# Kernel tuning notes

Hardware: AMD Instinct MI355X
Metric: run time of the kernel (lower is better)

## Reference

```python
import jax, jax.numpy as jnp
import numpy as np

NUM_EMBEDDINGS = 1024
EMBEDDING_DIM = 256
BETA = 0.25


def setup_inputs() -> dict:
    key = jax.random.key(0)
    k1, k2 = jax.random.split(key)
    inputs = jax.random.normal(k1, (32, EMBEDDING_DIM, 64, 64), dtype=jnp.float32)
    # codebook init: uniform(-1/K, 1/K), matching nn.Embedding init in the module
    embedding = jax.random.uniform(
        k2, (NUM_EMBEDDINGS, EMBEDDING_DIM), dtype=jnp.float32,
        minval=-1.0 / NUM_EMBEDDINGS, maxval=1.0 / NUM_EMBEDDINGS)
    return {"inputs": inputs, "embedding": embedding, "beta": BETA}


def reference(inputs, embedding, beta):
    # inputs: [B, D, H, W] -> [B, H, W, D]
    x = jnp.transpose(inputs, (0, 2, 3, 1))
    in_shape = x.shape
    flat = x.reshape(-1, embedding.shape[1])  # [N, D]
    dist = (jnp.sum(flat * flat, axis=1, keepdims=True)
            + jnp.sum(embedding * embedding, axis=1)
            - 2.0 * flat @ embedding.T)
    codebook_indices = jnp.argmin(dist, axis=1)  # [N]
    quantized = embedding[codebook_indices].reshape(in_shape)  # [B,H,W,D]
    sg = jax.lax.stop_gradient
    e_latent_loss = beta * jnp.mean((sg(quantized) - x) ** 2)
    q_latent_loss = jnp.mean((quantized - sg(x)) ** 2)
    loss = e_latent_loss + q_latent_loss
    # straight-through estimator
    quantized_st = x + sg(quantized - x)
    return loss, jnp.transpose(quantized_st, (0, 3, 1, 2))
```

## Files before the change

### kernel.cpp

```cpp
#include <hip/hip_runtime.h>


#define DIN 256

typedef __attribute__((ext_vector_type(8))) short short8;
typedef __attribute__((ext_vector_type(4))) float float4v;
typedef __attribute__((ext_vector_type(4))) unsigned short ushort4v;

static __device__ __forceinline__ unsigned short f2bf(float f) {
  unsigned int u = __float_as_uint(f);
  unsigned int r = (u + 0x7fffu + ((u >> 16) & 1u)) >> 16;
  return (unsigned short)r;
}

__global__ void vq_prep(const float* __restrict__ e,
                        unsigned short* __restrict__ e_pre,
                        float* __restrict__ norms) {
  int wave = threadIdx.x >> 6, lane = threadIdx.x & 63;
  int k = blockIdx.x * 4 + wave;
  const float4v* src = (const float4v*)(e + k * DIN);
  float4v v = src[lane];
  float ss = v[0]*v[0] + v[1]*v[1] + v[2]*v[2] + v[3]*v[3];
  ushort4v pk;
  pk[0] = f2bf(v[0]); pk[1] = f2bf(v[1]); pk[2] = f2bf(v[2]); pk[3] = f2bf(v[3]);
  int t = k >> 5, kL = k & 31;
  int cc = lane >> 1, half = lane & 1;
  int s = cc ^ (kL & 7);
  *(ushort4v*)(e_pre + t * 8192 + kL * 256 + s * 8 + half * 4) = pk;
  #pragma unroll
  for (int m = 1; m < 64; m <<= 1) ss += __shfl_xor(ss, m, 64);
  if (lane == 0) norms[k] = ss;
}

#define BARRIER_RAW() do { asm volatile("" ::: "memory"); \
  __builtin_amdgcn_s_barrier(); asm volatile("" ::: "memory"); } while (0)

__global__ void __launch_bounds__(256, 2)
vq_main(const float* __restrict__ xin, const float* __restrict__ e_fp,
        const unsigned short* __restrict__ e_pre,
        const float* __restrict__ norms,
        float* __restrict__ out, float* __restrict__ loss_acc) {
  __shared__ char smem[65536];
  float* qs  = (float*)smem;
  float* nrm = (float*)(smem + 32768);
  float* xna = (float*)(smem + 36864);
  int*   fi  = (int*)(smem + 37888);
  float* prt = (float*)(smem + 38912);

  const int tid  = threadIdx.x;
  const int wave = tid >> 6, lane = tid & 63;
  const int m16  = lane & 15, quad = lane >> 4;
  const int line0 = blockIdx.x * 4;
  const int line  = line0 + wave;
  const float* xl = xin + (line >> 6) * 1048576 + (line & 63) * 64;

  auto stage = [&](int t, int buf) {
    const char* src = (const char*)e_pre + t * 16384;
    char* dst = smem + buf * 16384;
    #pragma unroll
    for (int j = 0; j < 4; ++j) {
      int off = j * 4096 + tid * 16;
      __builtin_amdgcn_global_load_lds(
          (const __attribute__((address_space(1))) unsigned int*)(src + off),
          (__attribute__((address_space(3))) unsigned int*)(dst + off),
          16, 0, 0);
    }
  };
  stage(0, 0);

  nrm[tid]       = norms[tid];
  nrm[tid + 256] = norms[tid + 256];
  nrm[tid + 512] = norms[tid + 512];
  nrm[tid + 768] = norms[tid + 768];

  short8 areg[32];
  {
    float ssq[4] = {0.0f, 0.0f, 0.0f, 0.0f};
    #pragma unroll
    for (int i = 0; i < 4; ++i) {
      const float* p = xl + i * 16 + m16;
      #pragma unroll
      for (int kk = 0; kk < 8; ++kk) {
        int dbase = kk * 32 + quad * 8;
        short8 pk;
        #pragma unroll
        for (int ii = 0; ii < 8; ++ii) {
          float xv = p[(dbase + ii) * 4096];
          ssq[i] += xv * xv;
          pk[ii] = (short)f2bf(xv);
        }
        areg[i * 8 + kk] = pk;
      }
    }
    #pragma unroll
    for (int i = 0; i < 4; ++i) {
      float s = ssq[i];
      s += __shfl_xor(s, 16, 64);
      s += __shfl_xor(s, 32, 64);
      if (quad == 0) xna[wave * 64 + i * 16 + m16] = s;
    }
  }

  float bestv[4][4];
  int   besti[4][4];
  #pragma unroll
  for (int i = 0; i < 4; ++i)
    #pragma unroll
    for (int r = 0; r < 4; ++r) { bestv[i][r] = INFINITY; besti[i][r] = 0; }

  for (int t = 0; t < 32; ++t) {
    if (t < 31) {
      stage(t + 1, (t + 1) & 1);
      asm volatile("s_waitcnt vmcnt(4)" ::: "memory");
    } else {
      asm volatile("s_waitcnt vmcnt(0)" ::: "memory");
    }
    BARRIER_RAW();
    const unsigned short* eb = (const unsigned short*)(smem + (t & 1) * 16384);
    #pragma unroll
    for (int j = 0; j < 2; ++j) {
      int cL = j * 16 + m16;
      float4v a0 = (float4v)(0.0f), a1 = (float4v)(0.0f);
      float4v a2 = (float4v)(0.0f), a3 = (float4v)(0.0f);
      #pragma unroll
      for (int kk = 0; kk < 8; ++kk) {
        short8 bfr = *(const short8*)(eb + cL * 256 + 8 * ((kk * 4 + quad) ^ (cL & 7)));
        a0 = __builtin_amdgcn_mfma_f32_16x16x32_bf16(areg[kk],      bfr, a0, 0, 0, 0);
        a1 = __builtin_amdgcn_mfma_f32_16x16x32_bf16(areg[8 + kk],  bfr, a1, 0, 0, 0);
        a2 = __builtin_amdgcn_mfma_f32_16x16x32_bf16(areg[16 + kk], bfr, a2, 0, 0, 0);
        a3 = __builtin_amdgcn_mfma_f32_16x16x32_bf16(areg[24 + kk], bfr, a3, 0, 0, 0);
      }
      int col = t * 32 + cL;
      float nj = nrm[col];
      #pragma unroll
      for (int r = 0; r < 4; ++r) {
        float s0 = nj - 2.0f * a0[r];
        if (s0 < bestv[0][r]) { bestv[0][r] = s0; besti[0][r] = col; }
        float s1 = nj - 2.0f * a1[r];
        if (s1 < bestv[1][r]) { bestv[1][r] = s1; besti[1][r] = col; }
        float s2 = nj - 2.0f * a2[r];
        if (s2 < bestv[2][r]) { bestv[2][r] = s2; besti[2][r] = col; }
        float s3 = nj - 2.0f * a3[r];
        if (s3 < bestv[3][r]) { bestv[3][r] = s3; besti[3][r] = col; }
      }
    }
    BARRIER_RAW();
  }

  #pragma unroll
  for (int msk = 1; msk <= 8; msk <<= 1) {
    #pragma unroll
    for (int i = 0; i < 4; ++i)
      #pragma unroll
      for (int r = 0; r < 4; ++r) {
        float ov = __shfl_xor(bestv[i][r], msk, 64);
        int   oi = __shfl_xor(besti[i][r], msk, 64);
        if (ov < bestv[i][r] || (ov == bestv[i][r] && oi < besti[i][r])) {
          bestv[i][r] = ov; besti[i][r] = oi;
        }
      }
  }

  float lsum = 0.0f;
  if (m16 == 0) {
    #pragma unroll
    for (int i = 0; i < 4; ++i)
      #pragma unroll
      for (int r = 0; r < 4; ++r) {
        int row = wave * 64 + i * 16 + quad * 4 + r;
        fi[row] = besti[i][r];
        lsum += bestv[i][r] + xna[row];
      }
  }
  #pragma unroll
  for (int msk = 1; msk < 64; msk <<= 1) lsum += __shfl_xor(lsum, msk, 64);
  if (lane == 0) prt[wave] = lsum;
  __syncthreads();
  if (tid == 0)
    atomicAdd(loss_acc, prt[0] + prt[1] + prt[2] + prt[3]);

  const int b0 = line0 >> 6, h0 = line0 & 63;
  float* out1 = out + 1 + b0 * 1048576 + h0 * 64;
  const int myidx = fi[tid];
  const float* er = e_fp + myidx * 256;
  __syncthreads();
  for (int q = 0; q < 4; ++q) {
    if (q) __syncthreads();
    #pragma unroll
    for (int c = 0; c < 16; ++c) {
      float4v qv = *(const float4v*)(er + q * 64 + c * 4);
      qs[(c * 4 + 0) * 256 + tid] = qv[0];
      qs[(c * 4 + 1) * 256 + tid] = qv[1];
      qs[(c * 4 + 2) * 256 + tid] = qv[2];
      qs[(c * 4 + 3) * 256 + tid] = qv[3];
    }
    __syncthreads();
    #pragma unroll
    for (int it = 0; it < 16; ++it) {
      int dl = it * 4 + wave;
      float4v ov = *(const float4v*)(qs + dl * 256 + lane * 4);
      *(float4v*)(out1 + (q * 64 + dl) * 4096 + lane * 4) = ov;
    }
  }
}

__global__ void vq_fin(const float* __restrict__ loss_acc,
                       const float* __restrict__ beta,
                       float* __restrict__ out) {
  out[0] = (1.0f + beta[0]) * loss_acc[0] / 33554432.0f;
}

extern "C" void kernel_launch(void* const* d_in, const int* in_sizes, int n_in,
                              void* d_out, int out_size, void* d_ws, size_t ws_size,
                              hipStream_t stream) {
  const float* xin  = (const float*)d_in[0];
  const float* emb  = (const float*)d_in[1];
  const float* beta = (const float*)d_in[2];
  float* out = (float*)d_out;
  float* loss_acc = (float*)d_ws;
  float* norms = (float*)((char*)d_ws + 4096);
  unsigned short* e_pre = (unsigned short*)((char*)d_ws + 8192);

  hipMemsetAsync(d_ws, 0, 4, stream);
  vq_prep<<<256, 256, 0, stream>>>(emb, e_pre, norms);
  vq_main<<<512, 256, 0, stream>>>(xin, emb, e_pre, norms, out, loss_acc);
  vq_fin<<<1, 1, 0, stream>>>(loss_acc, beta, out);
}
```

Measured before the change: 360.7 us.

## Split gather into separate scatter kernel using transposed codebook in LDS

Splits the fused argmin/gather kernel in two. The argmin kernel now loads x with coalesced per-lane reads, restages it through a swizzled LDS buffer to build the MFMA fragments, and writes the chosen indices to a global buffer. A new scatter kernel keeps a transposed fp32 codebook slice in LDS and writes the NCHW output directly, with no per-row gather. This targets the strided x loads and the LDS transpose stage for the output, at the cost of an extra launch and an index round-trip through global memory.

```diff
diff --git a/kernel.cpp b/kernel.cpp
--- a/kernel.cpp
+++ b/kernel.cpp
@@ -6,6 +6,7 @@
 typedef __attribute__((ext_vector_type(8))) short short8;
 typedef __attribute__((ext_vector_type(4))) float float4v;
 typedef __attribute__((ext_vector_type(4))) unsigned short ushort4v;
+typedef __attribute__((ext_vector_type(4))) int int4v;
 
 static __device__ __forceinline__ unsigned short f2bf(float f) {
   unsigned int u = __float_as_uint(f);
@@ -15,7 +16,8 @@
 
 __global__ void vq_prep(const float* __restrict__ e,
                         unsigned short* __restrict__ e_pre,
-                        float* __restrict__ norms) {
+                        float* __restrict__ norms,
+                        float* __restrict__ eT) {
   int wave = threadIdx.x >> 6, lane = threadIdx.x & 63;
   int k = blockIdx.x * 4 + wave;
   const float4v* src = (const float4v*)(e + k * DIN);
@@ -28,6 +30,9 @@
   int s = cc ^ (kL & 7);
   *(ushort4v*)(e_pre + t * 8192 + kL * 256 + s * 8 + half * 4) = pk;
   #pragma unroll
+  for (int ii = 0; ii < 4; ++ii)
+    eT[(lane * 4 + ii) * 1024 + k] = v[ii];
+  #pragma unroll
   for (int m = 1; m < 64; m <<= 1) ss += __shfl_xor(ss, m, 64);
   if (lane == 0) norms[k] = ss;
 }
@@ -36,22 +41,18 @@
   __builtin_amdgcn_s_barrier(); asm volatile("" ::: "memory"); } while (0)
 
 __global__ void __launch_bounds__(256, 2)
-vq_main(const float* __restrict__ xin, const float* __restrict__ e_fp,
-        const unsigned short* __restrict__ e_pre,
-        const float* __restrict__ norms,
-        float* __restrict__ out, float* __restrict__ loss_acc) {
-  __shared__ char smem[65536];
-  float* qs  = (float*)smem;
-  float* nrm = (float*)(smem + 32768);
-  float* xna = (float*)(smem + 36864);
-  int*   fi  = (int*)(smem + 37888);
-  float* prt = (float*)(smem + 38912);
+vq_argmin(const float* __restrict__ xin,
+          const unsigned short* __restrict__ e_pre,
+          const float* __restrict__ norms,
+          int* __restrict__ fig, float* __restrict__ loss_acc) {
+  __shared__ __align__(16) char smem[69648];
+  float* nrm = (float*)(smem + 65536);
+  float* prt = (float*)(smem + 69632);
 
   const int tid  = threadIdx.x;
   const int wave = tid >> 6, lane = tid & 63;
   const int m16  = lane & 15, quad = lane >> 4;
-  const int line0 = blockIdx.x * 4;
-  const int line  = line0 + wave;
+  const int line = blockIdx.x * 4 + wave;
   const float* xl = xin + (line >> 6) * 1048576 + (line & 63) * 64;
 
   auto stage = [&](int t, int buf) {
@@ -68,38 +69,35 @@
   };
   stage(0, 0);
 
-  nrm[tid]       = norms[tid];
-  nrm[tid + 256] = norms[tid + 256];
-  nrm[tid + 512] = norms[tid + 512];
-  nrm[tid + 768] = norms[tid + 768];
-
+  *(float4v*)(nrm + tid * 4) = *(const float4v*)(norms + tid * 4);
+
+  unsigned short* xsw = (unsigned short*)(smem + 32768 + wave * 8192);
   short8 areg[32];
-  {
-    float ssq[4] = {0.0f, 0.0f, 0.0f, 0.0f};
-    #pragma unroll
-    for (int i = 0; i < 4; ++i) {
-      const float* p = xl + i * 16 + m16;
-      #pragma unroll
-      for (int kk = 0; kk < 8; ++kk) {
-        int dbase = kk * 32 + quad * 8;
-        short8 pk;
-        #pragma unroll
-        for (int ii = 0; ii < 8; ++ii) {
-          float xv = p[(dbase + ii) * 4096];
-          ssq[i] += xv * xv;
-          pk[ii] = (short)f2bf(xv);
-        }
-        areg[i * 8 + kk] = pk;
-      }
-    }
-    #pragma unroll
-    for (int i = 0; i < 4; ++i) {
-      float s = ssq[i];
-      s += __shfl_xor(s, 16, 64);
-      s += __shfl_xor(s, 32, 64);
-      if (quad == 0) xna[wave * 64 + i * 16 + m16] = s;
-    }
-  }
+  float ssq = 0.0f;
+  #pragma unroll
+  for (int q = 0; q < 4; ++q) {
+    #pragma unroll
+    for (int c = 0; c < 8; ++c) {
+      short8 pk;
+      #pragma unroll
+      for (int ii = 0; ii < 8; ++ii) {
+        float xv = xl[(q * 64 + c * 8 + ii) * 4096 + lane];
+        ssq += xv * xv;
+        pk[ii] = (short)f2bf(xv);
+      }
+      *(short8*)(xsw + lane * 64 + ((c ^ (lane & 7)) * 8)) = pk;
+    }
+    #pragma unroll
+    for (int i = 0; i < 4; ++i)
+      #pragma unroll
+      for (int kl = 0; kl < 2; ++kl) {
+        int r = i * 16 + m16;
+        int cl = kl * 4 + quad;
+        areg[i * 8 + q * 2 + kl] =
+            *(short8*)(xsw + r * 64 + ((cl ^ (r & 7)) * 8));
+      }
+  }
+  asm volatile("s_waitcnt lgkmcnt(0)" ::: "memory");
 
   float bestv[4][4];
   int   besti[4][4];
@@ -161,15 +159,15 @@
       }
   }
 
-  float lsum = 0.0f;
+  float lsum = ssq;
   if (m16 == 0) {
     #pragma unroll
     for (int i = 0; i < 4; ++i)
       #pragma unroll
       for (int r = 0; r < 4; ++r) {
-        int row = wave * 64 + i * 16 + quad * 4 + r;
-        fi[row] = besti[i][r];
-        lsum += bestv[i][r] + xna[row];
+        int row = i * 16 + quad * 4 + r;
+        fig[line * 64 + row] = besti[i][r];
+        lsum += bestv[i][r];
       }
   }
   #pragma unroll
@@ -178,28 +176,50 @@
   __syncthreads();
   if (tid == 0)
     atomicAdd(loss_acc, prt[0] + prt[1] + prt[2] + prt[3]);
-
-  const int b0 = line0 >> 6, h0 = line0 & 63;
-  float* out1 = out + 1 + b0 * 1048576 + h0 * 64;
-  const int myidx = fi[tid];
-  const float* er = e_fp + myidx * 256;
+}
+
+__global__ void __launch_bounds__(256, 3)
+vq_scatter(const float* __restrict__ eT, const int* __restrict__ fig,
+           float* __restrict__ out) {
+  __shared__ __align__(16) char smem[49152];
+  float* eTl = (float*)smem;
+  int*   fil = (int*)(smem + 32768);
+  const int tid = threadIdx.x;
+  const int b = blockIdx.x >> 5, dc = blockIdx.x & 31;
+
+  const char* s0 = (const char*)eT + dc * 32768;
+  #pragma unroll
+  for (int j = 0; j < 8; ++j) {
+    int off = j * 4096 + tid * 16;
+    __builtin_amdgcn_global_load_lds(
+        (const __attribute__((address_space(1))) unsigned int*)(s0 + off),
+        (__attribute__((address_space(3))) unsigned int*)(smem + off),
+        16, 0, 0);
+  }
+  const char* s1 = (const char*)(fig + b * 4096);
+  #pragma unroll
+  for (int j = 0; j < 4; ++j) {
+    int off = j * 4096 + tid * 16;
+    __builtin_amdgcn_global_load_lds(
+        (const __attribute__((address_space(1))) unsigned int*)(s1 + off),
+        (__attribute__((address_space(3))) unsigned int*)(smem + 32768 + off),
+        16, 0, 0);
+  }
+  asm volatile("s_waitcnt vmcnt(0)" ::: "memory");
   __syncthreads();
-  for (int q = 0; q < 4; ++q) {
-    if (q) __syncthreads();
-    #pragma unroll
-    for (int c = 0; c < 16; ++c) {
-      float4v qv = *(const float4v*)(er + q * 64 + c * 4);
-      qs[(c * 4 + 0) * 256 + tid] = qv[0];
-      qs[(c * 4 + 1) * 256 + tid] = qv[1];
-      qs[(c * 4 + 2) * 256 + tid] = qv[2];
-      qs[(c * 4 + 3) * 256 + tid] = qv[3];
-    }
-    __syncthreads();
-    #pragma unroll
-    for (int it = 0; it < 16; ++it) {
-      int dl = it * 4 + wave;
-      float4v ov = *(const float4v*)(qs + dl * 256 + lane * 4);
-      *(float4v*)(out1 + (q * 64 + dl) * 4096 + lane * 4) = ov;
+
+  float* ob = out + 1 + b * 1048576 + dc * 8 * 4096;
+  for (int ro = 0; ro < 4; ++ro) {
+    int p = ro * 1024 + tid * 4;
+    int4v idx = *(const int4v*)(fil + p);
+    #pragma unroll
+    for (int d = 0; d < 8; ++d) {
+      float4v v;
+      v[0] = eTl[d * 1024 + idx[0]];
+      v[1] = eTl[d * 1024 + idx[1]];
+      v[2] = eTl[d * 1024 + idx[2]];
+      v[3] = eTl[d * 1024 + idx[3]];
+      *(float4v*)(ob + d * 4096 + p) = v;
     }
   }
 }
@@ -220,9 +240,12 @@
   float* loss_acc = (float*)d_ws;
   float* norms = (float*)((char*)d_ws + 4096);
   unsigned short* e_pre = (unsigned short*)((char*)d_ws + 8192);
+  float* eT = (float*)((char*)d_ws + 532480);
+  int* fig = (int*)((char*)d_ws + 1581056);
 
   hipMemsetAsync(d_ws, 0, 4, stream);
-  vq_prep<<<256, 256, 0, stream>>>(emb, e_pre, norms);
-  vq_main<<<512, 256, 0, stream>>>(xin, emb, e_pre, norms, out, loss_acc);
+  vq_prep<<<256, 256, 0, stream>>>(emb, e_pre, norms, eT);
+  vq_argmin<<<512, 256, 0, stream>>>(xin, e_pre, norms, fig, loss_acc);
+  vq_scatter<<<1024, 256, 0, stream>>>(eT, fig, out);
   vq_fin<<<1, 1, 0, stream>>>(loss_acc, beta, out);
 }
```

Result: slower. 422.4 us (+17.1%).
